# Optimization experiments

Measured on AMD Instinct MI355X. Metric: run time of the kernel, lower is better.

## Reference

```python
import jax, jax.numpy as jnp
import numpy as np

NUM_HEADS = 16
MASK_VAL = -1e6  # d2l masked_softmax fill value


def setup_inputs() -> dict:
    key = jax.random.key(0)
    ks = jax.random.split(key, 8)
    B, S, D = 4, 1024, 1024
    scale = 1.0 / np.sqrt(D)
    inp = {
        "queries": jax.random.normal(ks[0], (B, S, D), dtype=jnp.float32),
        "keys": jax.random.normal(ks[1], (B, S, D), dtype=jnp.float32),
        "values": jax.random.normal(ks[2], (B, S, D), dtype=jnp.float32),
        "valid_lens": jax.random.randint(ks[3], (B,), 1, S + 1, dtype=jnp.int32),
        "W_q": jax.random.normal(ks[4], (D, D), dtype=jnp.float32) * scale,
        "W_k": jax.random.normal(ks[5], (D, D), dtype=jnp.float32) * scale,
        "W_v": jax.random.normal(ks[6], (D, D), dtype=jnp.float32) * scale,
        "W_o": jax.random.normal(ks[7], (D, D), dtype=jnp.float32) * scale,
    }
    return inp


def _split_heads(x, H):
    # [B, S, D] -> [B, H, S, d]
    B, S, D = x.shape
    return x.reshape(B, S, H, D // H).transpose(0, 2, 1, 3)


def reference(queries, keys, values, valid_lens, W_q, W_k, W_v, W_o):
    H = NUM_HEADS
    B, Sq, D = queries.shape
    Sk = keys.shape[1]
    d = D // H

    q = _split_heads(queries @ W_q.T, H)  # [B, H, Sq, d]
    k = _split_heads(keys @ W_k.T, H)     # [B, H, Sk, d]
    v = _split_heads(values @ W_v.T, H)   # [B, H, Sk, d]

    scores = jnp.einsum("bhqd,bhkd->bhqk", q, k) / jnp.sqrt(jnp.float32(d))
    # masked_softmax: mask key positions >= valid_len (per batch row)
    mask = jnp.arange(Sk)[None, None, None, :] < valid_lens[:, None, None, None]
    scores = jnp.where(mask, scores, MASK_VAL)
    attn = jax.nn.softmax(scores, axis=-1)  # dropout=0.0 -> identity

    out = jnp.einsum("bhqk,bhkd->bhqd", attn, v)  # [B, H, Sq, d]
    out = out.transpose(0, 2, 1, 3).reshape(B, Sq, D)
    return out @ W_o.T
```

## Files before the change

### kernel.cpp

```cpp
#include <hip/hip_runtime.h>

typedef unsigned short ushort_t;
typedef unsigned int uint32;
typedef __attribute__((ext_vector_type(8))) short short8;
typedef __attribute__((ext_vector_type(4))) float float4v;
typedef __attribute__((ext_vector_type(4))) unsigned short ushort4v;

#define NEG_INF (-__builtin_inff())

__device__ __forceinline__ ushort_t f2bf(float f) {
  uint32 u = __float_as_uint(f);
  u += 0x7fffu + ((u >> 16) & 1u);
  return (ushort_t)(u >> 16);
}

__device__ __forceinline__ void glds16(const void* g, void* l) {
  __builtin_amdgcn_global_load_lds(
      (__attribute__((address_space(1))) const void*)g,
      (__attribute__((address_space(3))) void*)l, 16, 0, 0);
}

struct CvtW {
  const float* in[4];
  ushort_t* out[4];
};

__global__ __launch_bounds__(256) void cvt_w_kernel(CvtW a) {
  const float* in = a.in[blockIdx.y];
  ushort_t* out = a.out[blockIdx.y];
  int i = blockIdx.x * 256 + threadIdx.x;
  float4v v = ((const float4v*)in)[i];
  ushort4v o;
  o.x = f2bf(v.x);
  o.y = f2bf(v.y);
  o.z = f2bf(v.z);
  o.w = f2bf(v.w);
  ((ushort4v*)out)[i] = o;
}

struct ProjArgs {
  const float* A[3];
  const ushort_t* B[3];
  ushort_t* C[3];
};

__global__ __launch_bounds__(256) void gemm_proj(ProjArgs pa, int M, int N,
                                                 int K) {
  __shared__ __align__(16) ushort_t Al[2][128][32];
  __shared__ __align__(16) ushort_t Bl[2][128][32];
  const int orig = blockIdx.x + (blockIdx.y << 3) + (blockIdx.z << 8);
  const int swz = (orig & 7) * 96 + (orig >> 3);
  const int bn = (swz & 7) * 128;
  const int bm = ((swz >> 3) & 31) * 128;
  const int z = swz >> 8;
  const float* A = pa.A[z];
  const ushort_t* B = pa.B[z];
  ushort_t* C = pa.C[z];
  const int tid = threadIdx.x;
  const int w = tid >> 6, lane = tid & 63;
  const int l15 = lane & 15, lhi = lane >> 4;
  const int wm = (w >> 1) * 64, wn = (w & 1) * 64;

  float4v zero4 = {0.f, 0.f, 0.f, 0.f};
  float4v acc[4][4];
  for (int i = 0; i < 4; i++)
    for (int j = 0; j < 4; j++) acc[i][j] = zero4;

  const int sr = tid >> 2;
  const int sc = tid & 3;
  const int ssw = sc ^ ((sr >> 1) & 3);
  const ushort_t* gb = B + (size_t)(bn + sr) * K + ssw * 8;
  char* lBb = (char*)&Bl[0][0][0];
  const int wb = w * 1024;
  const float* gaf = A + (size_t)(bm + sr) * K + sc * 8;
  const int rsw8 = (lhi ^ ((l15 >> 1) & 3)) * 8;
  const int NT = K / 32;

  glds16(gb, lBb + wb);
  glds16(gb + (size_t)64 * K, lBb + 4096 + wb);
#pragma unroll
  for (int rep = 0; rep < 2; rep++) {
    const float* p = gaf + (size_t)rep * 64 * K;
    float4v u0 = ((const float4v*)p)[0];
    float4v u1 = ((const float4v*)p)[1];
    short8 sv;
    sv[0] = (short)f2bf(u0.x);
    sv[1] = (short)f2bf(u0.y);
    sv[2] = (short)f2bf(u0.z);
    sv[3] = (short)f2bf(u0.w);
    sv[4] = (short)f2bf(u1.x);
    sv[5] = (short)f2bf(u1.y);
    sv[6] = (short)f2bf(u1.z);
    sv[7] = (short)f2bf(u1.w);
    *(short8*)&Al[0][rep * 64 + sr][ssw * 8] = sv;
  }
  __syncthreads();

  int cur = 0;
  for (int t = 0; t < NT; ++t) {
    const int ktn = (t + 1) * 32;
    const bool pf = (t + 1 < NT);
    float4v pu0[2], pu1[2];
    if (pf) {
      char* lBn = lBb + (cur ^ 1) * 8192;
      glds16(gb + ktn, lBn + wb);
      glds16(gb + (size_t)64 * K + ktn, lBn + 4096 + wb);
#pragma unroll
      for (int rep = 0; rep < 2; rep++) {
        const float* p = gaf + (size_t)rep * 64 * K + ktn;
        pu0[rep] = ((const float4v*)p)[0];
        pu1[rep] = ((const float4v*)p)[1];
      }
    }
    short8 af[4], bfr[4];
#pragma unroll
    for (int mi = 0; mi < 4; mi++)
      af[mi] = *(const short8*)&Al[cur][wm + mi * 16 + l15][rsw8];
#pragma unroll
    for (int ni = 0; ni < 4; ni++)
      bfr[ni] = *(const short8*)&Bl[cur][wn + ni * 16 + l15][rsw8];
#pragma unroll
    for (int mi = 0; mi < 4; mi++)
#pragma unroll
      for (int ni = 0; ni < 4; ni++)
        acc[mi][ni] = __builtin_amdgcn_mfma_f32_16x16x32_bf16(
            af[mi], bfr[ni], acc[mi][ni], 0, 0, 0);
    if (pf) {
#pragma unroll
      for (int rep = 0; rep < 2; rep++) {
        short8 sv;
        sv[0] = (short)f2bf(pu0[rep].x);
        sv[1] = (short)f2bf(pu0[rep].y);
        sv[2] = (short)f2bf(pu0[rep].z);
        sv[3] = (short)f2bf(pu0[rep].w);
        sv[4] = (short)f2bf(pu1[rep].x);
        sv[5] = (short)f2bf(pu1[rep].y);
        sv[6] = (short)f2bf(pu1[rep].z);
        sv[7] = (short)f2bf(pu1[rep].w);
        *(short8*)&Al[cur ^ 1][rep * 64 + sr][ssw * 8] = sv;
      }
    }
    __syncthreads();
    cur ^= 1;
  }

#pragma unroll
  for (int mi = 0; mi < 4; mi++)
#pragma unroll
    for (int ni = 0; ni < 4; ni++)
#pragma unroll
      for (int i = 0; i < 4; i++) {
        int row = bm + wm + mi * 16 + lhi * 4 + i;
        int col = bn + wn + ni * 16 + l15;
        C[(size_t)row * N + col] = f2bf(acc[mi][ni][i]);
      }
}

__global__ __launch_bounds__(256) void gemm_out(const ushort_t* __restrict__ A,
                                                const ushort_t* __restrict__ B,
                                                float* __restrict__ Cout, int M,
                                                int N, int K) {
  __shared__ __align__(16) ushort_t Al[2][128][32];
  __shared__ __align__(16) ushort_t Bl[2][128][32];
  const int orig = blockIdx.x + (blockIdx.y << 3);
  const int swz = (orig & 7) * 32 + (orig >> 3);
  const int bn = (swz & 7) * 128;
  const int bm = (swz >> 3) * 128;
  const int tid = threadIdx.x;
  const int w = tid >> 6, lane = tid & 63;
  const int l15 = lane & 15, lhi = lane >> 4;
  const int wm = (w >> 1) * 64, wn = (w & 1) * 64;

  float4v zero4 = {0.f, 0.f, 0.f, 0.f};
  float4v acc[4][4];
  for (int i = 0; i < 4; i++)
    for (int j = 0; j < 4; j++) acc[i][j] = zero4;

  const int sr = tid >> 2;
  const int sc = tid & 3;
  const int ssw = sc ^ ((sr >> 1) & 3);
  const ushort_t* ga = A + (size_t)(bm + sr) * K + ssw * 8;
  const ushort_t* gb = B + (size_t)(bn + sr) * K + ssw * 8;
  char* lAb = (char*)&Al[0][0][0];
  char* lBb = (char*)&Bl[0][0][0];
  const int wb = w * 1024;
  const int rsw8 = (lhi ^ ((l15 >> 1) & 3)) * 8;
  const int NT = K / 32;

  glds16(ga, lAb + wb);
  glds16(ga + (size_t)64 * K, lAb + 4096 + wb);
  glds16(gb, lBb + wb);
  glds16(gb + (size_t)64 * K, lBb + 4096 + wb);
  __syncthreads();

  int cur = 0;
  for (int t = 0; t < NT; ++t) {
    const int ktn = (t + 1) * 32;
    if (t + 1 < NT) {
      char* lAn = lAb + (cur ^ 1) * 8192;
      char* lBn = lBb + (cur ^ 1) * 8192;
      glds16(ga + ktn, lAn + wb);
      glds16(ga + (size_t)64 * K + ktn, lAn + 4096 + wb);
      glds16(gb + ktn, lBn + wb);
      glds16(gb + (size_t)64 * K + ktn, lBn + 4096 + wb);
    }
    short8 af[4], bfr[4];
#pragma unroll
    for (int mi = 0; mi < 4; mi++)
      af[mi] = *(const short8*)&Al[cur][wm + mi * 16 + l15][rsw8];
#pragma unroll
    for (int ni = 0; ni < 4; ni++)
      bfr[ni] = *(const short8*)&Bl[cur][wn + ni * 16 + l15][rsw8];
#pragma unroll
    for (int mi = 0; mi < 4; mi++)
#pragma unroll
      for (int ni = 0; ni < 4; ni++)
        acc[mi][ni] = __builtin_amdgcn_mfma_f32_16x16x32_bf16(
            af[mi], bfr[ni], acc[mi][ni], 0, 0, 0);
    __syncthreads();
    cur ^= 1;
  }

#pragma unroll
  for (int mi = 0; mi < 4; mi++)
#pragma unroll
    for (int ni = 0; ni < 4; ni++)
#pragma unroll
      for (int i = 0; i < 4; i++) {
        int row = bm + wm + mi * 16 + lhi * 4 + i;
        int col = bn + wn + ni * 16 + l15;
        Cout[(size_t)row * N + col] = acc[mi][ni][i];
      }
}

__global__ __launch_bounds__(256) void transpose_v_kernel(
    const ushort_t* __restrict__ Vp, ushort_t* __restrict__ Vt) {
  __shared__ ushort_t tile[64][65];
  const int bx = blockIdx.x;
  const int b = bx >> 8, h = (bx >> 4) & 15, c = bx & 15;
  const int t = threadIdx.x;
#pragma unroll
  for (int i = 0; i < 16; i++) {
    int id = i * 256 + t;
    int tok = id >> 6, dd = id & 63;
    tile[tok][dd] = Vp[(size_t)(b * 1024 + c * 64 + tok) * 1024 + h * 64 + dd];
  }
  __syncthreads();
#pragma unroll
  for (int i = 0; i < 16; i++) {
    int id = i * 256 + t;
    int dd = id >> 6, tok = id & 63;
    Vt[(size_t)((b * 16 + h) * 64 + dd) * 1024 + c * 64 + tok] = tile[tok][dd];
  }
}

__global__ __launch_bounds__(64) void attn_kernel(
    const ushort_t* __restrict__ Qp, const ushort_t* __restrict__ Kp,
    const ushort_t* __restrict__ Vt, const int* __restrict__ valid_lens,
    ushort_t* __restrict__ Ob) {
  __shared__ __align__(16) ushort_t Plds[16][72];
  const int lane = threadIdx.x & 63;
  const int l15 = lane & 15, lhi = lane >> 4;
  const int bx = blockIdx.x;
  const int b = bx >> 10;
  const int h = (bx >> 6) & 15;
  const int qt = bx & 63;
  const int qrow0 = qt * 16;
  const int vlen = valid_lens[b];

  short8 qf0, qf1;
  {
    const ushort_t* qp =
        Qp + (size_t)(b * 1024 + qrow0 + l15) * 1024 + h * 64 + lhi * 8;
    qf0 = *(const short8*)qp;
    qf1 = *(const short8*)(qp + 32);
  }
  float4v zero4 = {0.f, 0.f, 0.f, 0.f};
  float4v o[4] = {zero4, zero4, zero4, zero4};
  float m_i[4] = {NEG_INF, NEG_INF, NEG_INF, NEG_INF};
  float l_i[4] = {0.f, 0.f, 0.f, 0.f};

  const ushort_t* kh = Kp + (size_t)b * 1024 * 1024 + h * 64;
  const ushort_t* vh = Vt + (size_t)(b * 16 + h) * 64 * 1024;

  for (int kt = 0; kt < 16; kt++) {
    const int k0 = kt * 64;
    if (k0 >= vlen) break;

    float4v s[4];
#pragma unroll
    for (int n = 0; n < 4; n++) {
      const ushort_t* kp = kh + (size_t)(k0 + n * 16 + l15) * 1024 + lhi * 8;
      short8 kf0 = *(const short8*)kp;
      short8 kf1 = *(const short8*)(kp + 32);
      s[n] = __builtin_amdgcn_mfma_f32_16x16x32_bf16(qf0, kf0, zero4, 0, 0, 0);
      s[n] = __builtin_amdgcn_mfma_f32_16x16x32_bf16(qf1, kf1, s[n], 0, 0, 0);
    }
    float pm[4] = {NEG_INF, NEG_INF, NEG_INF, NEG_INF};
#pragma unroll
    for (int n = 0; n < 4; n++) {
      const bool ok = (k0 + n * 16 + l15) < vlen;
#pragma unroll
      for (int i = 0; i < 4; i++) {
        float v = s[n][i] * 0.125f;
        v = ok ? v : -1e6f;
        s[n][i] = v;
        pm[i] = fmaxf(pm[i], v);
      }
    }
#pragma unroll
    for (int d = 1; d < 16; d <<= 1)
#pragma unroll
      for (int i = 0; i < 4; i++) pm[i] = fmaxf(pm[i], __shfl_xor(pm[i], d, 64));

    float alpha[4], rs[4];
#pragma unroll
    for (int i = 0; i < 4; i++) {
      float mn = fmaxf(m_i[i], pm[i]);
      alpha[i] = __expf(m_i[i] - mn);
      m_i[i] = mn;
      rs[i] = 0.f;
    }
#pragma unroll
    for (int n = 0; n < 4; n++)
#pragma unroll
      for (int i = 0; i < 4; i++) {
        float p = __expf(s[n][i] - m_i[i]);
        s[n][i] = p;
        rs[i] += p;
      }
#pragma unroll
    for (int d = 1; d < 16; d <<= 1)
#pragma unroll
      for (int i = 0; i < 4; i++) rs[i] += __shfl_xor(rs[i], d, 64);
#pragma unroll
    for (int i = 0; i < 4; i++) l_i[i] = l_i[i] * alpha[i] + rs[i];
#pragma unroll
    for (int n = 0; n < 4; n++)
#pragma unroll
      for (int i = 0; i < 4; i++) o[n][i] *= alpha[i];

#pragma unroll
    for (int n = 0; n < 4; n++)
#pragma unroll
      for (int i = 0; i < 4; i++)
        Plds[lhi * 4 + i][n * 16 + l15] = f2bf(s[n][i]);

#pragma unroll
    for (int c = 0; c < 2; c++) {
      short8 pa = *(const short8*)&Plds[l15][c * 32 + lhi * 8];
      const ushort_t* vb = vh + k0 + c * 32 + lhi * 8;
#pragma unroll
      for (int n = 0; n < 4; n++) {
        short8 vf = *(const short8*)(vb + (size_t)(n * 16 + l15) * 1024);
        o[n] = __builtin_amdgcn_mfma_f32_16x16x32_bf16(pa, vf, o[n], 0, 0, 0);
      }
    }
  }

#pragma unroll
  for (int n = 0; n < 4; n++)
#pragma unroll
    for (int i = 0; i < 4; i++) {
      float vout = o[n][i] / l_i[i];
      Ob[(size_t)(b * 1024 + qrow0 + lhi * 4 + i) * 1024 + h * 64 + n * 16 +
         l15] = f2bf(vout);
    }
}

extern "C" void kernel_launch(void* const* d_in, const int* in_sizes, int n_in,
                              void* d_out, int out_size, void* d_ws,
                              size_t ws_size, hipStream_t stream) {
  (void)in_sizes;
  (void)n_in;
  (void)out_size;
  (void)ws_size;
  const float* q = (const float*)d_in[0];
  const float* k = (const float*)d_in[1];
  const float* v = (const float*)d_in[2];
  const int* vl = (const int*)d_in[3];
  const float* Wq = (const float*)d_in[4];
  const float* Wk = (const float*)d_in[5];
  const float* Wv = (const float*)d_in[6];
  const float* Wo = (const float*)d_in[7];
  float* out = (float*)d_out;
  char* ws = (char*)d_ws;
  const size_t MB = 1u << 20;

  ushort_t* wqb = (ushort_t*)(ws + 0 * MB);
  ushort_t* wkb = (ushort_t*)(ws + 2 * MB);
  ushort_t* wvb = (ushort_t*)(ws + 4 * MB);
  ushort_t* wob = (ushort_t*)(ws + 6 * MB);
  ushort_t* Qp = (ushort_t*)(ws + 8 * MB);
  ushort_t* Kp = (ushort_t*)(ws + 16 * MB);
  ushort_t* Vp = (ushort_t*)(ws + 24 * MB);
  ushort_t* Vtp = (ushort_t*)(ws + 32 * MB);
  ushort_t* Ob = Vp;

  CvtW cw;
  cw.in[0] = Wq;
  cw.in[1] = Wk;
  cw.in[2] = Wv;
  cw.in[3] = Wo;
  cw.out[0] = wqb;
  cw.out[1] = wkb;
  cw.out[2] = wvb;
  cw.out[3] = wob;
  cvt_w_kernel<<<dim3(1024, 4), 256, 0, stream>>>(cw);

  ProjArgs pa;
  pa.A[0] = q;
  pa.A[1] = k;
  pa.A[2] = v;
  pa.B[0] = wqb;
  pa.B[1] = wkb;
  pa.B[2] = wvb;
  pa.C[0] = Qp;
  pa.C[1] = Kp;
  pa.C[2] = Vp;
  gemm_proj<<<dim3(8, 32, 3), 256, 0, stream>>>(pa, 4096, 1024, 1024);

  transpose_v_kernel<<<1024, 256, 0, stream>>>(Vp, Vtp);
  attn_kernel<<<4096, 64, 0, stream>>>(Qp, Kp, Vtp, vl, Ob);
  gemm_out<<<dim3(8, 32), 256, 0, stream>>>(Ob, wob, out, 4096, 1024, 1024);
}
```

Baseline: 225.0 us.

## Deepen A-operand prefetch in projection GEMM with manual waitcnt barriers

Rewrites the projection GEMM main loop as a 2x-unrolled software pipeline. The fp32 A tile is loaded into registers two k-steps ahead while the bf16 B tile is fetched one step ahead straight into LDS. Plain __syncthreads is replaced by explicit s_waitcnt vmcnt/lgkmcnt plus s_barrier, so the A global loads can stay in flight across the barrier. K is made a compile-time constant. The goal is to hide global load latency behind the MFMA work, at the cost of more registers and fragile hand-counted vmcnt values.

```diff
diff --git a/kernel.cpp b/kernel.cpp
--- a/kernel.cpp
+++ b/kernel.cpp
@@ -12,6 +12,19 @@
   uint32 u = __float_as_uint(f);
   u += 0x7fffu + ((u >> 16) & 1u);
   return (ushort_t)(u >> 16);
+}
+
+__device__ __forceinline__ short8 cvt8(float4v u0, float4v u1) {
+  short8 sv;
+  sv[0] = (short)f2bf(u0.x);
+  sv[1] = (short)f2bf(u0.y);
+  sv[2] = (short)f2bf(u0.z);
+  sv[3] = (short)f2bf(u0.w);
+  sv[4] = (short)f2bf(u1.x);
+  sv[5] = (short)f2bf(u1.y);
+  sv[6] = (short)f2bf(u1.z);
+  sv[7] = (short)f2bf(u1.w);
+  return sv;
 }
 
 __device__ __forceinline__ void glds16(const void* g, void* l) {
@@ -44,8 +57,9 @@
   ushort_t* C[3];
 };
 
-__global__ __launch_bounds__(256) void gemm_proj(ProjArgs pa, int M, int N,
-                                                 int K) {
+__global__ __launch_bounds__(256) void gemm_proj(ProjArgs pa, int M, int N) {
+  constexpr int K = 1024;
+  constexpr int NT = K / 32;
   __shared__ __align__(16) ushort_t Al[2][128][32];
   __shared__ __align__(16) ushort_t Bl[2][128][32];
   const int orig = blockIdx.x + (blockIdx.y << 3) + (blockIdx.z << 8);
@@ -70,79 +84,86 @@
   const int sc = tid & 3;
   const int ssw = sc ^ ((sr >> 1) & 3);
   const ushort_t* gb = B + (size_t)(bn + sr) * K + ssw * 8;
+  const float* gaf = A + (size_t)(bm + sr) * K + sc * 8;
   char* lBb = (char*)&Bl[0][0][0];
   const int wb = w * 1024;
-  const float* gaf = A + (size_t)(bm + sr) * K + sc * 8;
   const int rsw8 = (lhi ^ ((l15 >> 1) & 3)) * 8;
-  const int NT = K / 32;
-
-  glds16(gb, lBb + wb);
-  glds16(gb + (size_t)64 * K, lBb + 4096 + wb);
-#pragma unroll
-  for (int rep = 0; rep < 2; rep++) {
-    const float* p = gaf + (size_t)rep * 64 * K;
-    float4v u0 = ((const float4v*)p)[0];
-    float4v u1 = ((const float4v*)p)[1];
-    short8 sv;
-    sv[0] = (short)f2bf(u0.x);
-    sv[1] = (short)f2bf(u0.y);
-    sv[2] = (short)f2bf(u0.z);
-    sv[3] = (short)f2bf(u0.w);
-    sv[4] = (short)f2bf(u1.x);
-    sv[5] = (short)f2bf(u1.y);
-    sv[6] = (short)f2bf(u1.z);
-    sv[7] = (short)f2bf(u1.w);
-    *(short8*)&Al[0][rep * 64 + sr][ssw * 8] = sv;
-  }
-  __syncthreads();
-
-  int cur = 0;
-  for (int t = 0; t < NT; ++t) {
-    const int ktn = (t + 1) * 32;
-    const bool pf = (t + 1 < NT);
-    float4v pu0[2], pu1[2];
-    if (pf) {
-      char* lBn = lBb + (cur ^ 1) * 8192;
-      glds16(gb + ktn, lBn + wb);
-      glds16(gb + (size_t)64 * K + ktn, lBn + 4096 + wb);
-#pragma unroll
-      for (int rep = 0; rep < 2; rep++) {
-        const float* p = gaf + (size_t)rep * 64 * K + ktn;
-        pu0[rep] = ((const float4v*)p)[0];
-        pu1[rep] = ((const float4v*)p)[1];
-      }
-    }
-    short8 af[4], bfr[4];
-#pragma unroll
-    for (int mi = 0; mi < 4; mi++)
-      af[mi] = *(const short8*)&Al[cur][wm + mi * 16 + l15][rsw8];
-#pragma unroll
-    for (int ni = 0; ni < 4; ni++)
-      bfr[ni] = *(const short8*)&Bl[cur][wn + ni * 16 + l15][rsw8];
-#pragma unroll
-    for (int mi = 0; mi < 4; mi++)
-#pragma unroll
-      for (int ni = 0; ni < 4; ni++)
-        acc[mi][ni] = __builtin_amdgcn_mfma_f32_16x16x32_bf16(
-            af[mi], bfr[ni], acc[mi][ni], 0, 0, 0);
-    if (pf) {
-#pragma unroll
-      for (int rep = 0; rep < 2; rep++) {
-        short8 sv;
-        sv[0] = (short)f2bf(pu0[rep].x);
-        sv[1] = (short)f2bf(pu0[rep].y);
-        sv[2] = (short)f2bf(pu0[rep].z);
-        sv[3] = (short)f2bf(pu0[rep].w);
-        sv[4] = (short)f2bf(pu1[rep].x);
-        sv[5] = (short)f2bf(pu1[rep].y);
-        sv[6] = (short)f2bf(pu1[rep].z);
-        sv[7] = (short)f2bf(pu1[rep].w);
-        *(short8*)&Al[cur ^ 1][rep * 64 + sr][ssw * 8] = sv;
-      }
-    }
-    __syncthreads();
-    cur ^= 1;
-  }
+
+  float4v e00, e01, e10, e11;
+  float4v o00, o01, o10, o11;
+
+#define LOADA(d00, d01, d10, d11, KT)          \
+  do {                                         \
+    const float* p0 = gaf + (KT);              \
+    d00 = ((const float4v*)p0)[0];             \
+    d01 = ((const float4v*)p0)[1];             \
+    const float* p1 = gaf + (size_t)64 * K + (KT); \
+    d10 = ((const float4v*)p1)[0];             \
+    d11 = ((const float4v*)p1)[1];             \
+  } while (0)
+
+#define STOREA(BUF, s00, s01, s10, s11)                   \
+  do {                                                    \
+    *(short8*)&Al[BUF][sr][ssw * 8] = cvt8(s00, s01);     \
+    *(short8*)&Al[BUF][64 + sr][ssw * 8] = cvt8(s10, s11); \
+  } while (0)
+
+#define GLDSB(BUF, KT)                                           \
+  do {                                                           \
+    glds16(gb + (KT), lBb + (BUF)*8192 + wb);                    \
+    glds16(gb + (size_t)64 * K + (KT), lBb + (BUF)*8192 + 4096 + wb); \
+  } while (0)
+
+#define MFMAS(BUF)                                                        \
+  do {                                                                    \
+    short8 af[4], bfr[4];                                                 \
+    _Pragma("unroll") for (int mi = 0; mi < 4; mi++)                      \
+        af[mi] = *(const short8*)&Al[BUF][wm + mi * 16 + l15][rsw8];      \
+    _Pragma("unroll") for (int ni = 0; ni < 4; ni++)                      \
+        bfr[ni] = *(const short8*)&Bl[BUF][wn + ni * 16 + l15][rsw8];     \
+    _Pragma("unroll") for (int mi = 0; mi < 4; mi++)                      \
+        _Pragma("unroll") for (int ni = 0; ni < 4; ni++) acc[mi][ni] =    \
+        __builtin_amdgcn_mfma_f32_16x16x32_bf16(af[mi], bfr[ni],          \
+                                                acc[mi][ni], 0, 0, 0);    \
+  } while (0)
+
+#define BAR(N_IMM)                                                     \
+  do {                                                                 \
+    asm volatile("s_waitcnt vmcnt(" #N_IMM ") lgkmcnt(0)" ::: "memory"); \
+    __builtin_amdgcn_s_barrier();                                      \
+    __builtin_amdgcn_sched_barrier(0);                                 \
+  } while (0)
+
+  LOADA(e00, e01, e10, e11, 0);
+  GLDSB(0, 0);
+  LOADA(o00, o01, o10, o11, 32);
+  STOREA(0, e00, e01, e10, e11);
+  BAR(4);
+
+  for (int t = 0; t < NT - 2; t += 2) {
+    GLDSB(1, (t + 1) * 32);
+    LOADA(e00, e01, e10, e11, (t + 2) * 32);
+    MFMAS(0);
+    STOREA(1, o00, o01, o10, o11);
+    BAR(4);
+    GLDSB(0, (t + 2) * 32);
+    LOADA(o00, o01, o10, o11, (t + 3) * 32);
+    MFMAS(1);
+    STOREA(0, e00, e01, e10, e11);
+    BAR(4);
+  }
+
+  GLDSB(1, (NT - 1) * 32);
+  MFMAS(0);
+  STOREA(1, o00, o01, o10, o11);
+  BAR(0);
+  MFMAS(1);
+
+#undef LOADA
+#undef STOREA
+#undef GLDSB
+#undef MFMAS
+#undef BAR
 
 #pragma unroll
   for (int mi = 0; mi < 4; mi++)
@@ -418,7 +439,7 @@
   pa.C[0] = Qp;
   pa.C[1] = Kp;
   pa.C[2] = Vp;
-  gemm_proj<<<dim3(8, 32, 3), 256, 0, stream>>>(pa, 4096, 1024, 1024);
+  gemm_proj<<<dim3(8, 32, 3), 256, 0, stream>>>(pa, 4096, 1024);
 
   transpose_v_kernel<<<1024, 256, 0, stream>>>(Vp, Vtp);
   attn_kernel<<<4096, 64, 0, stream>>>(Qp, Kp, Vtp, vl, Ob);
```

Measured after the change: 237.9 us. 1.06x slower.
